# Optimization experiments

Hardware: AMD Instinct MI355X
Metric: run time of the kernel (lower is better)

Reference implementation:

```python
import jax, jax.numpy as jnp
import numpy as np
import math

B, T, C = 2, 2048, 1024
H = 16
D = C // H

def setup_inputs() -> dict:
    key = jax.random.key(0)
    k1, k2, k3, k4, k5 = jax.random.split(key, 5)
    scale = 0.02
    return {
        "x": jax.random.normal(k1, (B, T, C), dtype=jnp.float32),
        "w_attn": jax.random.normal(k2, (3 * C, C), dtype=jnp.float32) * scale,
        "b_attn": jax.random.normal(k3, (3 * C,), dtype=jnp.float32) * scale,
        "w_proj": jax.random.normal(k4, (C, C), dtype=jnp.float32) * scale,
        "b_proj": jax.random.normal(k5, (C,), dtype=jnp.float32) * scale,
    }

def reference(x, w_attn, b_attn, w_proj, b_proj):
    b, t, c = x.shape
    # c_attn: torch Linear -> x @ W.T + b, output [b, t, 3c]
    qkv = jnp.einsum('btc,fc->btf', x, w_attn) + b_attn
    # einops 'b t (a h d) -> a b h t d' with a=3, h=H
    qkv = qkv.reshape(b, t, 3, H, D).transpose(2, 0, 3, 1, 4)
    q, k, v = qkv[0], qkv[1], qkv[2]  # each [b, h, t, d]
    att = jnp.einsum('bhtd,bhsd->bhts', q, k) * (1.0 / math.sqrt(D))
    # causal mask: positions s > t are masked
    mask = jnp.tril(jnp.ones((t, t), dtype=bool))
    att = jnp.where(mask[None, None, :, :], att, jnp.float32(-jnp.inf))
    att = jax.nn.softmax(att, axis=-1)
    y = jnp.einsum('bhts,bhsd->bhtd', att, v)  # [b, h, t, d]
    y = y.transpose(0, 2, 1, 3).reshape(b, t, c)
    return jnp.einsum('btc,fc->btf', y, w_proj) + b_proj
```

## Files before the change

### kernel.cpp

```cpp
#include <hip/hip_runtime.h>
#include <stdint.h>

typedef unsigned short u16;
typedef __attribute__((ext_vector_type(8))) __bf16 bvec8;
typedef __attribute__((ext_vector_type(4))) float f32x4;

__device__ __forceinline__ u16 f32_to_bf16(float f) {
    uint32_t u = __float_as_uint(f);
    u += 0x7fffu + ((u >> 16) & 1u);
    return (u16)(u >> 16);
}

__device__ __forceinline__ void gl2lds16(const u16* g, u16* l) {
    void* gnc = const_cast<void*>((const void*)g);
    __builtin_amdgcn_global_load_lds(
        (__attribute__((address_space(1))) uint32_t*)gnc,
        (__attribute__((address_space(3))) uint32_t*)((void*)l),
        16, 0, 0);
}

__global__ __launch_bounds__(256) void cvt3(
    const float* __restrict__ a, int na4, const float* __restrict__ b, int nb4,
    const float* __restrict__ c, int nc4,
    u16* __restrict__ oa, u16* __restrict__ ob, u16* __restrict__ oc)
{
    int i = blockIdx.x * 256 + threadIdx.x;
    const float* src; u16* dst; int off;
    if (i < na4)             { src = a; dst = oa; off = i; }
    else if (i < na4 + nb4)  { src = b; dst = ob; off = i - na4; }
    else if (i < na4 + nb4 + nc4) { src = c; dst = oc; off = i - na4 - nb4; }
    else return;
    float4 v = ((const float4*)src)[off];
    ushort4 o;
    o.x = f32_to_bf16(v.x); o.y = f32_to_bf16(v.y);
    o.z = f32_to_bf16(v.z); o.w = f32_to_bf16(v.w);
    ((ushort4*)dst)[off] = o;
}

template <int BNt, bool OUT_BF16>
__global__ __launch_bounds__(256) void gemm_bt_bias(
    const u16* __restrict__ A, const u16* __restrict__ B,
    const float* __restrict__ bias, void* __restrict__ Cv,
    int M, int N, int K)
{
    constexpr int NT = BNt / 32;
    __shared__ __attribute__((aligned(16))) u16 As[128 * 32];
    __shared__ __attribute__((aligned(16))) u16 Bs[BNt * 32];

    const int tid = threadIdx.x, wave = tid >> 6, lane = tid & 63;
    const int col = lane & 15, quad = lane >> 4;
    const int m0 = blockIdx.y * 128, n0 = blockIdx.x * BNt;
    const int wm = (wave >> 1) * 64, wn = (wave & 1) * (BNt / 2);
    const int srow = lane >> 2, schunk = lane & 3;
    const u16* Ag = A + (size_t)(m0 + wave * 32) * K;

    f32x4 acc[4][NT];
#pragma unroll
    for (int i = 0; i < 4; i++)
#pragma unroll
        for (int j = 0; j < NT; j++) acc[i][j] = f32x4{0.f, 0.f, 0.f, 0.f};

    for (int k0 = 0; k0 < K; k0 += 32) {
        __syncthreads();
        gl2lds16(Ag + (size_t)(srow)      * K + k0 + schunk * 8, &As[(wave * 2 + 0) * 512]);
        gl2lds16(Ag + (size_t)(16 + srow) * K + k0 + schunk * 8, &As[(wave * 2 + 1) * 512]);
        if constexpr (BNt == 128) {
            const u16* Bg = B + (size_t)(n0 + wave * 32) * K;
            gl2lds16(Bg + (size_t)(srow)      * K + k0 + schunk * 8, &Bs[(wave * 2 + 0) * 512]);
            gl2lds16(Bg + (size_t)(16 + srow) * K + k0 + schunk * 8, &Bs[(wave * 2 + 1) * 512]);
        } else {
            const u16* Bg = B + (size_t)(n0 + wave * 16) * K;
            gl2lds16(Bg + (size_t)(srow)      * K + k0 + schunk * 8, &Bs[wave * 512]);
        }
        __syncthreads();

        bvec8 af[4], bfv[NT];
#pragma unroll
        for (int mt = 0; mt < 4; mt++)  af[mt]  = *(const bvec8*)&As[(wm + mt * 16 + col) * 32 + quad * 8];
#pragma unroll
        for (int nt = 0; nt < NT; nt++) bfv[nt] = *(const bvec8*)&Bs[(wn + nt * 16 + col) * 32 + quad * 8];
#pragma unroll
        for (int mt = 0; mt < 4; mt++)
#pragma unroll
            for (int nt = 0; nt < NT; nt++)
                acc[mt][nt] = __builtin_amdgcn_mfma_f32_16x16x32_bf16(af[mt], bfv[nt], acc[mt][nt], 0, 0, 0);
    }

#pragma unroll
    for (int mt = 0; mt < 4; mt++) {
#pragma unroll
        for (int r = 0; r < 4; r++) {
            const int m = m0 + wm + mt * 16 + quad * 4 + r;
#pragma unroll
            for (int nt = 0; nt < NT; nt++) {
                const int n = n0 + wn + nt * 16 + col;
                float v = acc[mt][nt][r] + bias[n];
                if (OUT_BF16) ((u16*)Cv)[(size_t)m * N + n] = f32_to_bf16(v);
                else          ((float*)Cv)[(size_t)m * N + n] = v;
            }
        }
    }
}

__global__ __launch_bounds__(256) void transpose_v(const u16* __restrict__ qkv,
                                                   u16* __restrict__ vT)
{
    __shared__ u16 Ts[64 * 74];
    const int tid = threadIdx.x;
    const int t0 = blockIdx.x * 64, h = blockIdx.y, b = blockIdx.z;
    const u16* src = qkv + (size_t)b * 2048 * 3072 + 2048 + h * 64;
#pragma unroll
    for (int k2 = 0; k2 < 2; k2++) {
        int c = k2 * 256 + tid, tl = c >> 3, ch = c & 7;
        *(uint4*)&Ts[tl * 74 + ch * 8] = *(const uint4*)(src + (size_t)(t0 + tl) * 3072 + ch * 8);
    }
    __syncthreads();
    u16* dst = vT + (size_t)((b * 16 + h) * 64) * 2048;
#pragma unroll
    for (int k2 = 0; k2 < 2; k2++) {
        int c = k2 * 256 + tid, d = c >> 3, tch = c & 7;
        u16 tmp[8];
#pragma unroll
        for (int j2 = 0; j2 < 8; j2++) tmp[j2] = Ts[(tch * 8 + j2) * 74 + d];
        *(uint4*)&dst[(size_t)d * 2048 + t0 + tch * 8] = *(const uint4*)tmp;
    }
}

__global__ __launch_bounds__(256) void attn_kernel(const u16* __restrict__ qkv,
                                                   const u16* __restrict__ vT,
                                                   u16* __restrict__ Y)
{
    __shared__ __attribute__((aligned(16))) u16 Qs[64 * 64];
    __shared__ __attribute__((aligned(16))) u16 Ks[2][64 * 64];
    __shared__ __attribute__((aligned(16))) u16 Vs[2][64 * 64];
    __shared__ __attribute__((aligned(16))) u16 Ps[4 * 16 * 72];

    const int tid = threadIdx.x, wave = tid >> 6, lane = tid & 63;
    const int col = lane & 15, quad = lane >> 4;

    const int g = blockIdx.x;
    const int b = g >> 4, h = g & 15;
    const int s_idx = blockIdx.y;

    const u16* qb = qkv + (size_t)b * 2048 * 3072;
    const u16* vb = vT + (size_t)g * 64 * 2048;

    const int c0 = wave * 64 + lane, c1 = 256 + c0;
    const int r0 = c0 >> 3, p0 = c0 & 7, r1 = c1 >> 3, p1 = c1 & 7;
    const int sw0 = (p0 ^ (r0 & 7)) * 8, sw1 = (p1 ^ (r1 & 7)) * 8;

    const int tloc = wave * 16 + quad * 4;

#pragma unroll
    for (int phase = 0; phase < 2; ++phase) {
        const int qt = phase ? (31 - s_idx) : s_idx;
        const int q0 = qt * 64;

        __syncthreads();
        gl2lds16(qb + (size_t)(q0 + r0) * 3072 + h * 64 + sw0, &Qs[wave * 512]);
        gl2lds16(qb + (size_t)(q0 + r1) * 3072 + h * 64 + sw1, &Qs[2048 + wave * 512]);
        __syncthreads();

        const int qrow = wave * 16 + col;
        bvec8 qf0 = *(const bvec8*)&Qs[qrow * 64 + ((quad       ^ (qrow & 7)) * 8)];
        bvec8 qf1 = *(const bvec8*)&Qs[qrow * 64 + (((4 + quad) ^ (qrow & 7)) * 8)];

        float l_acc[4] = {0.f, 0.f, 0.f, 0.f};
        f32x4 o[4];
#pragma unroll
        for (int d = 0; d < 4; d++) o[d] = f32x4{0.f, 0.f, 0.f, 0.f};

        {
            gl2lds16(qb + (size_t)(r0) * 3072 + 1024 + h * 64 + sw0, &Ks[0][wave * 512]);
            gl2lds16(qb + (size_t)(r1) * 3072 + 1024 + h * 64 + sw1, &Ks[0][2048 + wave * 512]);
            gl2lds16(vb + (size_t)r0 * 2048 + sw0, &Vs[0][wave * 512]);
            gl2lds16(vb + (size_t)r1 * 2048 + sw1, &Vs[0][2048 + wave * 512]);
        }

        for (int kt = 0; kt <= qt; ++kt) {
            const int cur = kt & 1;
            if (kt < qt) {
                const int s0n = (kt + 1) * 64;
                const int nb2 = cur ^ 1;
                gl2lds16(qb + (size_t)(s0n + r0) * 3072 + 1024 + h * 64 + sw0, &Ks[nb2][wave * 512]);
                gl2lds16(qb + (size_t)(s0n + r1) * 3072 + 1024 + h * 64 + sw1, &Ks[nb2][2048 + wave * 512]);
                gl2lds16(vb + (size_t)r0 * 2048 + s0n + sw0, &Vs[nb2][wave * 512]);
                gl2lds16(vb + (size_t)r1 * 2048 + s0n + sw1, &Vs[nb2][2048 + wave * 512]);
                asm volatile("s_waitcnt vmcnt(4)" ::: "memory");
            } else {
                asm volatile("s_waitcnt vmcnt(0)" ::: "memory");
            }
            asm volatile("s_barrier" ::: "memory");

            f32x4 sv[4];
#pragma unroll
            for (int nt = 0; nt < 4; nt++) {
                const int krow = nt * 16 + col;
                bvec8 kf0 = *(const bvec8*)&Ks[cur][krow * 64 + ((quad       ^ (krow & 7)) * 8)];
                bvec8 kf1 = *(const bvec8*)&Ks[cur][krow * 64 + (((4 + quad) ^ (krow & 7)) * 8)];
                sv[nt] = f32x4{0.f, 0.f, 0.f, 0.f};
                sv[nt] = __builtin_amdgcn_mfma_f32_16x16x32_bf16(qf0, kf0, sv[nt], 0, 0, 0);
                sv[nt] = __builtin_amdgcn_mfma_f32_16x16x32_bf16(qf1, kf1, sv[nt], 0, 0, 0);
            }

            const bool diag = (kt == qt);
            u16* pw = &Ps[wave * 16 * 72];
#pragma unroll
            for (int nt = 0; nt < 4; nt++) {
#pragma unroll
                for (int r = 0; r < 4; r++) {
                    float p = __expf(sv[nt][r] * 0.125f);
                    if (diag && (nt * 16 + col) > (tloc + r)) p = 0.f;
                    l_acc[r] += p;
                    pw[(quad * 4 + r) * 72 + nt * 16 + col] = f32_to_bf16(p);
                }
            }

#pragma unroll
            for (int ks = 0; ks < 2; ks++) {
                bvec8 pf = *(const bvec8*)&Ps[wave * 16 * 72 + col * 72 + ks * 32 + quad * 8];
#pragma unroll
                for (int d = 0; d < 4; d++) {
                    const int vrow = d * 16 + col;
                    bvec8 vf = *(const bvec8*)&Vs[cur][vrow * 64 + (((ks * 4 + quad) ^ (vrow & 7)) * 8)];
                    o[d] = __builtin_amdgcn_mfma_f32_16x16x32_bf16(pf, vf, o[d], 0, 0, 0);
                }
            }
            asm volatile("s_barrier" ::: "memory");
        }

#pragma unroll
        for (int r = 0; r < 4; r++) {
            float s = l_acc[r];
            s += __shfl_xor(s, 1); s += __shfl_xor(s, 2);
            s += __shfl_xor(s, 4); s += __shfl_xor(s, 8);
            const float inv = 1.0f / s;
            const int t = q0 + wave * 16 + quad * 4 + r;
#pragma unroll
            for (int d = 0; d < 4; d++)
                Y[(size_t)(b * 2048 + t) * 1024 + h * 64 + d * 16 + col] =
                    f32_to_bf16(o[d][r] * inv);
        }
    }
}

extern "C" void kernel_launch(void* const* d_in, const int* in_sizes, int n_in,
                              void* d_out, int out_size, void* d_ws, size_t ws_size,
                              hipStream_t stream) {
    const float* x      = (const float*)d_in[0];
    const float* w_attn = (const float*)d_in[1];
    const float* b_attn = (const float*)d_in[2];
    const float* w_proj = (const float*)d_in[3];
    const float* b_proj = (const float*)d_in[4];
    float* out = (float*)d_out;

    u16* xb  = (u16*)d_ws;
    u16* wab = xb  + (size_t)4096 * 1024;
    u16* wpb = wab + (size_t)3072 * 1024;
    u16* qkv = wpb + (size_t)1024 * 1024;
    u16* y   = qkv + (size_t)4096 * 3072;
    u16* vT  = xb;

    const int na4 = 4096 * 1024 / 4, nb4 = 3072 * 1024 / 4, nc4 = 1024 * 1024 / 4;
    cvt3<<<(na4 + nb4 + nc4 + 255) / 256, 256, 0, stream>>>(
        x, na4, w_attn, nb4, w_proj, nc4, xb, wab, wpb);

    dim3 g1(3072 / 128, 4096 / 128);
    gemm_bt_bias<128, true><<<g1, 256, 0, stream>>>(xb, wab, b_attn, qkv, 4096, 3072, 1024);

    dim3 gt(32, 16, 2);
    transpose_v<<<gt, 256, 0, stream>>>(qkv, vT);

    dim3 g2(32, 16, 1);
    attn_kernel<<<g2, 256, 0, stream>>>(qkv, vT, y);

    dim3 g3(1024 / 64, 4096 / 128);
    gemm_bt_bias<64, false><<<g3, 256, 0, stream>>>(y, wpb, b_proj, out, 4096, 1024, 1024);
}
```

Baseline: 192.0 us.

## Keep softmax probabilities in registers by transposing QK^T and permuting K rows

```diff
diff --git a/kernel.cpp b/kernel.cpp
--- a/kernel.cpp
+++ b/kernel.cpp
@@ -133,7 +133,6 @@
     __shared__ __attribute__((aligned(16))) u16 Qs[64 * 64];
     __shared__ __attribute__((aligned(16))) u16 Ks[2][64 * 64];
     __shared__ __attribute__((aligned(16))) u16 Vs[2][64 * 64];
-    __shared__ __attribute__((aligned(16))) u16 Ps[4 * 16 * 72];
 
     const int tid = threadIdx.x, wave = tid >> 6, lane = tid & 63;
     const int col = lane & 15, quad = lane >> 4;
@@ -148,8 +147,11 @@
     const int c0 = wave * 64 + lane, c1 = 256 + c0;
     const int r0 = c0 >> 3, p0 = c0 & 7, r1 = c1 >> 3, p1 = c1 & 7;
     const int sw0 = (p0 ^ (r0 & 7)) * 8, sw1 = (p1 ^ (r1 & 7)) * 8;
-
-    const int tloc = wave * 16 + quad * 4;
+    const int tau0 = (r0 & 32) | ((r0 & 12) << 1) | ((r0 & 16) >> 2) | (r0 & 3);
+    const int tau1 = (r1 & 32) | ((r1 & 12) << 1) | ((r1 & 16) >> 2) | (r1 & 3);
+
+    const int q8 = quad * 8;
+    const int qit = wave * 16 + col;
 
 #pragma unroll
     for (int phase = 0; phase < 2; ++phase) {
@@ -165,14 +167,14 @@
         bvec8 qf0 = *(const bvec8*)&Qs[qrow * 64 + ((quad       ^ (qrow & 7)) * 8)];
         bvec8 qf1 = *(const bvec8*)&Qs[qrow * 64 + (((4 + quad) ^ (qrow & 7)) * 8)];
 
-        float l_acc[4] = {0.f, 0.f, 0.f, 0.f};
+        float l_acc = 0.f;
         f32x4 o[4];
 #pragma unroll
         for (int d = 0; d < 4; d++) o[d] = f32x4{0.f, 0.f, 0.f, 0.f};
 
         {
-            gl2lds16(qb + (size_t)(r0) * 3072 + 1024 + h * 64 + sw0, &Ks[0][wave * 512]);
-            gl2lds16(qb + (size_t)(r1) * 3072 + 1024 + h * 64 + sw1, &Ks[0][2048 + wave * 512]);
+            gl2lds16(qb + (size_t)(tau0) * 3072 + 1024 + h * 64 + sw0, &Ks[0][wave * 512]);
+            gl2lds16(qb + (size_t)(tau1) * 3072 + 1024 + h * 64 + sw1, &Ks[0][2048 + wave * 512]);
             gl2lds16(vb + (size_t)r0 * 2048 + sw0, &Vs[0][wave * 512]);
             gl2lds16(vb + (size_t)r1 * 2048 + sw1, &Vs[0][2048 + wave * 512]);
         }
@@ -182,8 +184,8 @@
             if (kt < qt) {
                 const int s0n = (kt + 1) * 64;
                 const int nb2 = cur ^ 1;
-                gl2lds16(qb + (size_t)(s0n + r0) * 3072 + 1024 + h * 64 + sw0, &Ks[nb2][wave * 512]);
-                gl2lds16(qb + (size_t)(s0n + r1) * 3072 + 1024 + h * 64 + sw1, &Ks[nb2][2048 + wave * 512]);
+                gl2lds16(qb + (size_t)(s0n + tau0) * 3072 + 1024 + h * 64 + sw0, &Ks[nb2][wave * 512]);
+                gl2lds16(qb + (size_t)(s0n + tau1) * 3072 + 1024 + h * 64 + sw1, &Ks[nb2][2048 + wave * 512]);
                 gl2lds16(vb + (size_t)r0 * 2048 + s0n + sw0, &Vs[nb2][wave * 512]);
                 gl2lds16(vb + (size_t)r1 * 2048 + s0n + sw1, &Vs[nb2][2048 + wave * 512]);
                 asm volatile("s_waitcnt vmcnt(4)" ::: "memory");
@@ -199,42 +201,43 @@
                 bvec8 kf0 = *(const bvec8*)&Ks[cur][krow * 64 + ((quad       ^ (krow & 7)) * 8)];
                 bvec8 kf1 = *(const bvec8*)&Ks[cur][krow * 64 + (((4 + quad) ^ (krow & 7)) * 8)];
                 sv[nt] = f32x4{0.f, 0.f, 0.f, 0.f};
-                sv[nt] = __builtin_amdgcn_mfma_f32_16x16x32_bf16(qf0, kf0, sv[nt], 0, 0, 0);
-                sv[nt] = __builtin_amdgcn_mfma_f32_16x16x32_bf16(qf1, kf1, sv[nt], 0, 0, 0);
+                sv[nt] = __builtin_amdgcn_mfma_f32_16x16x32_bf16(kf0, qf0, sv[nt], 0, 0, 0);
+                sv[nt] = __builtin_amdgcn_mfma_f32_16x16x32_bf16(kf1, qf1, sv[nt], 0, 0, 0);
             }
 
             const bool diag = (kt == qt);
-            u16* pw = &Ps[wave * 16 * 72];
+            bvec8 pbv[2];
 #pragma unroll
             for (int nt = 0; nt < 4; nt++) {
 #pragma unroll
                 for (int r = 0; r < 4; r++) {
                     float p = __expf(sv[nt][r] * 0.125f);
-                    if (diag && (nt * 16 + col) > (tloc + r)) p = 0.f;
-                    l_acc[r] += p;
-                    pw[(quad * 4 + r) * 72 + nt * 16 + col] = f32_to_bf16(p);
+                    const int klog = 32 * (nt >> 1) + q8 + 4 * (nt & 1) + r;
+                    if (diag && klog > qit) p = 0.f;
+                    l_acc += p;
+                    pbv[nt >> 1][(nt & 1) * 4 + r] = (__bf16)p;
                 }
             }
 
 #pragma unroll
             for (int ks = 0; ks < 2; ks++) {
-                bvec8 pf = *(const bvec8*)&Ps[wave * 16 * 72 + col * 72 + ks * 32 + quad * 8];
 #pragma unroll
                 for (int d = 0; d < 4; d++) {
                     const int vrow = d * 16 + col;
                     bvec8 vf = *(const bvec8*)&Vs[cur][vrow * 64 + (((ks * 4 + quad) ^ (vrow & 7)) * 8)];
-                    o[d] = __builtin_amdgcn_mfma_f32_16x16x32_bf16(pf, vf, o[d], 0, 0, 0);
+                    o[d] = __builtin_amdgcn_mfma_f32_16x16x32_bf16(pbv[ks], vf, o[d], 0, 0, 0);
                 }
             }
             asm volatile("s_barrier" ::: "memory");
         }
 
+        float l = l_acc;
+        l += __shfl_xor(l, 16);
+        l += __shfl_xor(l, 32);
 #pragma unroll
         for (int r = 0; r < 4; r++) {
-            float s = l_acc[r];
-            s += __shfl_xor(s, 1); s += __shfl_xor(s, 2);
-            s += __shfl_xor(s, 4); s += __shfl_xor(s, 8);
-            const float inv = 1.0f / s;
+            const float lr = __shfl(l, quad * 4 + r);
+            const float inv = 1.0f / lr;
             const int t = q0 + wave * 16 + quad * 4 + r;
 #pragma unroll
             for (int d = 0; d < 4; d++)
```

New measurement: 182.4 us. -5.0%, faster.
